# Optimization experiments

Measured on AMD Instinct MI355X. Metric: run time of the kernel, lower is better.

## Reference

```python
import jax, jax.numpy as jnp
import numpy as np

# Mamba2 defaults (mamba_ssm): expand=2, headdim=64, d_conv=4, ngroups=1
D_MODEL, D_STATE, D_INNER, HEADDIM, D_CONV = 512, 64, 1024, 64, 4
NHEADS = D_INNER // HEADDIM  # 16
CONV_DIM = D_INNER + 2 * D_STATE  # 1152
D_IN_PROJ = 2 * D_INNER + 2 * D_STATE + NHEADS  # 2192
BATCH, SEQLEN = 2, 2048
RMS_EPS = 1.1920929e-07  # torch nn.RMSNorm eps=None -> fp32 machine eps
GNORM_EPS = 1e-5  # mamba_ssm RMSNormGated default


def _rms(t, w, eps):
    return t * jax.lax.rsqrt(jnp.mean(t * t, axis=-1, keepdims=True) + eps) * w


def _mamba2(u, in_w, conv_w, conv_b, dt_bias, A_log, Dp, gnorm_w, out_w):
    """Mamba2 block forward (ngroups=1). u: (b, l, d_model) -> (b, l, d_model)."""
    b, l, _ = u.shape
    zxbcdt = jnp.einsum('bld,ed->ble', u, in_w)  # (b, l, 2192)
    z = zxbcdt[..., :D_INNER]
    xBC = zxbcdt[..., D_INNER:D_INNER + CONV_DIM]
    dt = jax.nn.softplus(zxbcdt[..., -NHEADS:] + dt_bias)  # (b, l, h)
    # causal depthwise conv, kernel D_CONV, then SiLU
    xp = jnp.pad(xBC, ((0, 0), (D_CONV - 1, 0), (0, 0)))
    xBC = conv_b + sum(xp[:, i:i + l, :] * conv_w[:, i] for i in range(D_CONV))
    xBC = jax.nn.silu(xBC)
    x = xBC[..., :D_INNER].reshape(b, l, NHEADS, HEADDIM)
    Bm = xBC[..., D_INNER:D_INNER + D_STATE]  # (b, l, n)
    Cm = xBC[..., D_INNER + D_STATE:]         # (b, l, n)
    dA = jnp.exp(dt * (-jnp.exp(A_log)))      # (b, l, h), decay per head

    def step(h, inp):
        dA_t, dt_t, B_t, C_t, x_t = inp  # (b,h) (b,h) (b,n) (b,n) (b,h,p)
        h = h * dA_t[:, :, None, None] + jnp.einsum('bh,bhp,bn->bhpn', dt_t, x_t, B_t)
        y = jnp.einsum('bhpn,bn->bhp', h, C_t)
        return h, y

    h0 = jnp.zeros((b, NHEADS, HEADDIM, D_STATE), u.dtype)
    xs = (jnp.swapaxes(dA, 0, 1), jnp.swapaxes(dt, 0, 1), jnp.swapaxes(Bm, 0, 1),
          jnp.swapaxes(Cm, 0, 1), jnp.swapaxes(x, 0, 1))
    _, ys = jax.lax.scan(step, h0, xs)  # (l, b, h, p)
    y = jnp.swapaxes(ys, 0, 1) + x * Dp[None, None, :, None]
    y = y.reshape(b, l, D_INNER)
    # gated RMSNorm: norm(y * silu(z)) * weight
    y = y * jax.nn.silu(z)
    y = _rms(y, gnorm_w, GNORM_EPS)
    return jnp.einsum('bli,oi->blo', y, out_w)


def _layer(x, pos_emb, pixel_mask, norm_ssm_w, norm_ffn_w, ffn_w1, ffn_b1, ffn_w2, ffn_b2,
           f_in_w, f_conv_w, f_conv_b, f_dt_bias, f_A_log, f_D, f_gnorm_w, f_out_w,
           b_in_w, b_conv_w, b_conv_b, b_dt_bias, b_A_log, b_D, b_gnorm_w, b_out_w):
    si = _rms(x, norm_ssm_w, RMS_EPS) + pos_emb
    fwd = _mamba2(si, f_in_w, f_conv_w, f_conv_b, f_dt_bias, f_A_log, f_D, f_gnorm_w, f_out_w)
    bwd = jnp.flip(_mamba2(jnp.flip(si, 1), b_in_w, b_conv_w, b_conv_b, b_dt_bias,
                           b_A_log, b_D, b_gnorm_w, b_out_w), 1)
    ssm_out = (fwd + bwd) * pixel_mask[..., None]  # merge='add'
    x = x + ssm_out
    h = _rms(x, norm_ffn_w, RMS_EPS)
    h = jax.nn.gelu(h @ ffn_w1.T + ffn_b1, approximate=False)
    return x + (h @ ffn_w2.T + ffn_b2)


def setup_inputs() -> dict:
    key = jax.random.key(0)
    ks = jax.random.split(key, 16)
    f32 = jnp.float32
    inp = {}
    inp['x'] = jax.random.normal(ks[0], (BATCH, SEQLEN, D_MODEL), f32)
    inp['pos_emb'] = jax.random.normal(ks[1], (BATCH, SEQLEN, D_MODEL), f32) * 0.02
    inp['pixel_mask'] = jnp.ones((BATCH, SEQLEN), f32)
    inp['norm_ssm_w'] = jnp.ones((D_MODEL,), f32)
    inp['norm_ffn_w'] = jnp.ones((D_MODEL,), f32)
    d_ffn = 4 * D_MODEL
    inp['ffn_w1'] = jax.random.normal(ks[2], (d_ffn, D_MODEL), f32) * 0.02
    inp['ffn_b1'] = jnp.zeros((d_ffn,), f32)
    inp['ffn_w2'] = jax.random.normal(ks[3], (D_MODEL, d_ffn), f32) * 0.02
    inp['ffn_b2'] = jnp.zeros((D_MODEL,), f32)
    i = 4
    for pre in ('f', 'b'):
        inp[pre + '_in_w'] = jax.random.normal(ks[i], (D_IN_PROJ, D_MODEL), f32) * 0.02; i += 1
        inp[pre + '_conv_w'] = jax.random.uniform(ks[i], (CONV_DIM, D_CONV), f32, -0.5, 0.5); i += 1
        inp[pre + '_conv_b'] = jnp.zeros((CONV_DIM,), f32)
        dt0 = jnp.exp(jax.random.uniform(ks[i], (NHEADS,), f32) * (jnp.log(0.1) - jnp.log(0.001)) + jnp.log(0.001)); i += 1
        inp[pre + '_dt_bias'] = dt0 + jnp.log(-jnp.expm1(-dt0))  # inverse softplus
        inp[pre + '_A_log'] = jnp.log(jax.random.uniform(ks[i], (NHEADS,), f32, 1.0, 16.0)); i += 1
        inp[pre + '_D'] = jnp.ones((NHEADS,), f32)
        inp[pre + '_gnorm_w'] = jnp.ones((D_INNER,), f32)
        inp[pre + '_out_w'] = jax.random.normal(ks[i], (D_MODEL, D_INNER), f32) * 0.02; i += 1
    return inp


def reference(x, pos_emb, pixel_mask, norm_ssm_w, norm_ffn_w, ffn_w1, ffn_b1, ffn_w2, ffn_b2,
              f_in_w, f_conv_w, f_conv_b, f_dt_bias, f_A_log, f_D, f_gnorm_w, f_out_w,
              b_in_w, b_conv_w, b_conv_b, b_dt_bias, b_A_log, b_D, b_gnorm_w, b_out_w):
    return _layer(x, pos_emb, pixel_mask, norm_ssm_w, norm_ffn_w, ffn_w1, ffn_b1, ffn_w2, ffn_b2,
                  f_in_w, f_conv_w, f_conv_b, f_dt_bias, f_A_log, f_D, f_gnorm_w, f_out_w,
                  b_in_w, b_conv_w, b_conv_b, b_dt_bias, b_A_log, b_D, b_gnorm_w, b_out_w)
```

## Files before the change

kernel.cpp:

```cpp
#include <hip/hip_runtime.h>
#include <hip/hip_bf16.h>

typedef unsigned short u16;
typedef unsigned int u32;
typedef __bf16 bf16x8 __attribute__((ext_vector_type(8)));
typedef float f32x4 __attribute__((ext_vector_type(4)));

typedef __attribute__((address_space(1))) void gvoid_t;
typedef __attribute__((address_space(3))) void lvoid_t;
__device__ __forceinline__ void lds_cp16(void* lds, const void* g) {
    __builtin_amdgcn_global_load_lds((gvoid_t*)g, (lvoid_t*)lds, 16, 0, 0);
}

__device__ __forceinline__ float bf2f(u16 v) {
    u32 x = (u32)v << 16;
    return __builtin_bit_cast(float, x);
}
__device__ __forceinline__ u16 f2bf(float f) {
    return __builtin_bit_cast(u16, (__bf16)f);
}

__device__ __forceinline__ float block_sum_256(float v, float* red) {
    #pragma unroll
    for (int o = 32; o > 0; o >>= 1) v += __shfl_xor(v, o);
    int w = threadIdx.x >> 6;
    if ((threadIdx.x & 63) == 0) red[w] = v;
    __syncthreads();
    return red[0] + red[1] + red[2] + red[3];
}

__global__ void k_cvt_all(const float* __restrict__ f_inw, const float* __restrict__ b_inw,
                          const float* __restrict__ f_ow, const float* __restrict__ b_ow,
                          const float* __restrict__ w1, const float* __restrict__ w2,
                          u16* __restrict__ INWF, u16* __restrict__ INWB,
                          u16* __restrict__ OWF, u16* __restrict__ OWB,
                          u16* __restrict__ W1B, u16* __restrict__ W2B) {
    int i = blockIdx.x * 256 + threadIdx.x;
    if (i < 1179648) { int n = i >> 9; INWF[i] = (n < 2192) ? f2bf(f_inw[i]) : (u16)0; return; }
    i -= 1179648;
    if (i < 1179648) { int n = i >> 9; INWB[i] = (n < 2192) ? f2bf(b_inw[i]) : (u16)0; return; }
    i -= 1179648;
    if (i < 524288) { OWF[i] = f2bf(f_ow[i]); return; }
    i -= 524288;
    if (i < 524288) { OWB[i] = f2bf(b_ow[i]); return; }
    i -= 524288;
    if (i < 1048576) { W1B[i] = f2bf(w1[i]); return; }
    i -= 1048576;
    if (i < 1048576) W2B[i] = f2bf(w2[i]);
}

__global__ __launch_bounds__(256) void k_rms_pos(const float* __restrict__ x,
                                                 const float* __restrict__ pe,
                                                 const float* __restrict__ wrms,
                                                 u16* __restrict__ sib) {
    __shared__ float red[4];
    int row = blockIdx.x, t = threadIdx.x;
    size_t base = (size_t)row * 512 + t * 2;
    float2 xv = *(const float2*)(x + base);
    float ss = block_sum_256(xv.x * xv.x + xv.y * xv.y, red);
    float sc = rsqrtf(ss * (1.f / 512.f) + 1.1920929e-07f);
    float2 pv = *(const float2*)(pe + base);
    float2 wv = *(const float2*)(wrms + t * 2);
    sib[base] = f2bf(xv.x * sc * wv.x + pv.x);
    sib[base + 1] = f2bf(xv.y * sc * wv.y + pv.y);
}

__global__ __launch_bounds__(256) void k_gemm_in(
    const u16* __restrict__ A, const u16* __restrict__ W0, const u16* __restrict__ W1,
    u16* __restrict__ Z0, u16* __restrict__ Z1,
    u16* __restrict__ XB0, u16* __restrict__ XB1) {
    const int z = blockIdx.z;
    const u16* W = z ? W1 : W0;
    u16* Z = z ? Z1 : Z0;
    u16* XB = z ? XB1 : XB0;
    const int K = 512;

    __shared__ __align__(16) u16 As[128 * 32];
    __shared__ __align__(16) u16 Bs[128 * 32];

    const int t = threadIdx.x;
    const int lane = t & 63;
    const int w = t >> 6;
    const int m0 = blockIdx.y * 128;
    const int n0 = blockIdx.x * 128;
    const int wm = (w >> 1) * 64;
    const int wn = (w & 1) * 64;
    const int fr = lane & 15;
    const int fk = (lane >> 4) * 8;

    f32x4 acc[4][4];
    #pragma unroll
    for (int i = 0; i < 4; ++i)
        #pragma unroll
        for (int j = 0; j < 4; ++j) acc[i][j] = (f32x4){0.f, 0.f, 0.f, 0.f};

    for (int kt = 0; kt < K; kt += 32) {
        #pragma unroll
        for (int j = 0; j < 2; ++j) {
            int off16 = j * 256 + t;
            int row = off16 >> 2;
            int kc = (off16 & 3) * 8;
            int gm = m0 + row;
            if (z) gm = (gm & ~2047) | (2047 - (gm & 2047));
            lds_cp16(As + off16 * 8, A + (size_t)gm * K + kt + kc);
            lds_cp16(Bs + off16 * 8, W + (size_t)(n0 + row) * K + kt + kc);
        }
        __syncthreads();
        bf16x8 af[4], bfr[4];
        #pragma unroll
        for (int i = 0; i < 4; ++i) af[i] = *(const bf16x8*)(As + (wm + i * 16 + fr) * 32 + fk);
        #pragma unroll
        for (int i = 0; i < 4; ++i) bfr[i] = *(const bf16x8*)(Bs + (wn + i * 16 + fr) * 32 + fk);
        #pragma unroll
        for (int i = 0; i < 4; ++i)
            #pragma unroll
            for (int j = 0; j < 4; ++j)
                acc[i][j] = __builtin_amdgcn_mfma_f32_16x16x32_bf16(af[i], bfr[j], acc[i][j], 0, 0, 0);
        __syncthreads();
    }
    #pragma unroll
    for (int i = 0; i < 4; ++i) {
        int rbase = m0 + wm + i * 16 + (lane >> 4) * 4;
        #pragma unroll
        for (int j = 0; j < 4; ++j) {
            int c = n0 + wn + j * 16 + fr;
            #pragma unroll
            for (int r = 0; r < 4; ++r) {
                u16 v = f2bf(acc[i][j][r]);
                int m = rbase + r;
                if (c < 1024) Z[(size_t)m * 1024 + c] = v;
                else if (c < 2192) XB[(size_t)m * 1184 + (c - 1024)] = v;
            }
        }
    }
}

template <int EPI>
__global__ __launch_bounds__(256) void k_gemm64(
    const u16* __restrict__ A0, const u16* __restrict__ A1,
    const u16* __restrict__ W0, const u16* __restrict__ W1,
    u16* __restrict__ C0, u16* __restrict__ C1, int N, int K,
    const float* __restrict__ bias, float* __restrict__ outf) {
    const int z = blockIdx.z;
    const u16* A = (EPI == 3) ? A0 : (z ? A1 : A0);
    const u16* W = (EPI == 3) ? W0 : (z ? W1 : W0);
    u16* C = z ? C1 : C0;
    int kbeg = 0, kend = K;
    if (EPI == 3) { kbeg = z * (K >> 1); kend = kbeg + (K >> 1); }

    __shared__ __align__(16) u16 As[64 * 32];
    __shared__ __align__(16) u16 Bs[64 * 32];

    const int t = threadIdx.x;
    const int lane = t & 63;
    const int w = t >> 6;
    const int m0 = blockIdx.y * 64;
    const int n0 = blockIdx.x * 64;
    const int wm = (w >> 1) * 32;
    const int wn = (w & 1) * 32;
    const int fr = lane & 15;
    const int fk = (lane >> 4) * 8;

    f32x4 acc[2][2];
    #pragma unroll
    for (int i = 0; i < 2; ++i)
        #pragma unroll
        for (int j = 0; j < 2; ++j) acc[i][j] = (f32x4){0.f, 0.f, 0.f, 0.f};

    const int srow = t >> 2;
    const int skc = (t & 3) * 8;
    for (int kt = kbeg; kt < kend; kt += 32) {
        lds_cp16(As + t * 8, A + (size_t)(m0 + srow) * K + kt + skc);
        lds_cp16(Bs + t * 8, W + (size_t)(n0 + srow) * K + kt + skc);
        __syncthreads();
        bf16x8 af[2], bfr[2];
        #pragma unroll
        for (int i = 0; i < 2; ++i) af[i] = *(const bf16x8*)(As + (wm + i * 16 + fr) * 32 + fk);
        #pragma unroll
        for (int j = 0; j < 2; ++j) bfr[j] = *(const bf16x8*)(Bs + (wn + j * 16 + fr) * 32 + fk);
        #pragma unroll
        for (int i = 0; i < 2; ++i)
            #pragma unroll
            for (int j = 0; j < 2; ++j)
                acc[i][j] = __builtin_amdgcn_mfma_f32_16x16x32_bf16(af[i], bfr[j], acc[i][j], 0, 0, 0);
        __syncthreads();
    }
    #pragma unroll
    for (int i = 0; i < 2; ++i) {
        int rbase = m0 + wm + i * 16 + (lane >> 4) * 4;
        #pragma unroll
        for (int j = 0; j < 2; ++j) {
            int col = n0 + wn + j * 16 + fr;
            #pragma unroll
            for (int r = 0; r < 4; ++r) {
                int m = rbase + r;
                float v = acc[i][j][r];
                if (EPI == 0) {
                    C[(size_t)m * N + col] = f2bf(v);
                } else if (EPI == 1) {
                    float xg = v + bias[col];
                    C[(size_t)m * N + col] = f2bf(0.5f * xg * (1.f + erff(xg * 0.70710678118654752f)));
                } else {
                    atomicAdd(outf + (size_t)m * N + col, v);
                }
            }
        }
    }
}

__global__ __launch_bounds__(160) void k_conv(
    const u16* __restrict__ xb0, const u16* __restrict__ xb1,
    const float* __restrict__ cw0, const float* __restrict__ cb0,
    const float* __restrict__ dtb0, const float* __restrict__ al0,
    const float* __restrict__ cw1, const float* __restrict__ cb1,
    const float* __restrict__ dtb1, const float* __restrict__ al1,
    u16* __restrict__ xc0, u16* __restrict__ xc1,
    float* __restrict__ dtO0, float* __restrict__ dAO0,
    float* __restrict__ dtO1, float* __restrict__ dAO1) {
    int g = blockIdx.x;
    int dir = g >> 9;
    int row0 = (g & 511) * 8;
    const u16* xb = dir ? xb1 : xb0;
    const float* cw = dir ? cw1 : cw0;
    const float* cb = dir ? cb1 : cb0;
    const float* dtb = dir ? dtb1 : dtb0;
    const float* al = dir ? al1 : al0;
    u16* xc = dir ? xc1 : xc0;
    float* dtO = dir ? dtO1 : dtO0;
    float* dAO = dir ? dAO1 : dAO0;
    int tl0 = row0 & 2047;
    int rbatch = row0 - tl0;
    int t = threadIdx.x;
    if (t < 144) {
        int col = t * 8;
        float cwa[8][4];
        #pragma unroll
        for (int j = 0; j < 8; ++j) {
            float4 c4 = *(const float4*)(cw + (col + j) * 4);
            cwa[j][0] = c4.x; cwa[j][1] = c4.y; cwa[j][2] = c4.z; cwa[j][3] = c4.w;
        }
        float cbv[8];
        float4 cb0v = *(const float4*)(cb + col);
        float4 cb1v = *(const float4*)(cb + col + 4);
        cbv[0] = cb0v.x; cbv[1] = cb0v.y; cbv[2] = cb0v.z; cbv[3] = cb0v.w;
        cbv[4] = cb1v.x; cbv[5] = cb1v.y; cbv[6] = cb1v.z; cbv[7] = cb1v.w;
        uint4 win[4];
        win[0] = win[1] = win[2] = make_uint4(0, 0, 0, 0);
        #pragma unroll
        for (int i = 0; i < 3; ++i) {
            int tt = tl0 - 3 + i;
            if (tt >= 0) win[i] = *(const uint4*)(xb + (size_t)(rbatch + tt) * 1184 + col);
        }
        for (int s = 0; s < 8; ++s) {
            win[3] = *(const uint4*)(xb + (size_t)(rbatch + tl0 + s) * 1184 + col);
            const u16* w0 = (const u16*)&win[0];
            const u16* w1 = (const u16*)&win[1];
            const u16* w2 = (const u16*)&win[2];
            const u16* w3 = (const u16*)&win[3];
            u16 ov[8];
            #pragma unroll
            for (int j = 0; j < 8; ++j) {
                float a = cbv[j] + bf2f(w0[j]) * cwa[j][0] + bf2f(w1[j]) * cwa[j][1]
                        + bf2f(w2[j]) * cwa[j][2] + bf2f(w3[j]) * cwa[j][3];
                ov[j] = f2bf(a / (1.f + expf(-a)));
            }
            *(uint4*)(xc + (size_t)(row0 + s) * 1152 + col) = *(const uint4*)ov;
            win[0] = win[1]; win[1] = win[2]; win[2] = win[3];
        }
    } else if (t < 160) {
        int hh = t - 144;
        float nal = -expf(al[hh]);
        float dtbv = dtb[hh];
        for (int s = 0; s < 8; ++s) {
            int row = row0 + s;
            float v = bf2f(xb[(size_t)row * 1184 + 1152 + hh]) + dtbv;
            float sp = (v > 20.f) ? v : log1pf(expf(v));
            dtO[row * 16 + hh] = sp;
            dAO[row * 16 + hh] = nal * sp;
        }
    }
}

__global__ __launch_bounds__(256) void k_ssd_state(
    const u16* __restrict__ xc0, const float* __restrict__ dt0, const float* __restrict__ ld0,
    const u16* __restrict__ xc1, const float* __restrict__ dt1, const float* __restrict__ ld1,
    float* __restrict__ S, float* __restrict__ Aprod) {
    int blk = blockIdx.x;
    int c = blk & 31, h = (blk >> 5) & 15, b = (blk >> 9) & 1, dir = blk >> 10;
    const u16* xc = dir ? xc1 : xc0;
    const float* dtp = dir ? dt1 : dt0;
    const float* ldp = dir ? ld1 : ld0;
    const int t = threadIdx.x, w = t >> 6, lane = t & 63;
    const int fr = lane & 15, fk = (lane >> 4) * 8;

    __shared__ __align__(16) u16 sBt[64 * 72];
    __shared__ __align__(16) u16 sXp[64 * 72];
    __shared__ float ssc[64];
    size_t row0 = (size_t)b * 2048 + c * 64;

    if (t < 64) {
        float v = ldp[(row0 + t) * 16 + h];
        float dtv = dtp[(row0 + t) * 16 + h];
        #pragma unroll
        for (int o = 1; o < 64; o <<= 1) {
            float u = __shfl_up(v, o);
            if (lane >= o) v += u;
        }
        float last = __shfl(v, 63);
        ssc[t] = dtv * expf(last - v);
        if (t == 63) Aprod[blk] = expf(v);
    }
    __syncthreads();
    #pragma unroll
    for (int i2 = t; i2 < 512; i2 += 256) {
        int r = i2 >> 3, e8 = (i2 & 7) * 8;
        size_t rb = (row0 + r) * 1152;
        uint4 bv = *(const uint4*)(xc + rb + 1024 + e8);
        uint4 xv = *(const uint4*)(xc + rb + h * 64 + e8);
        const u16* bs = (const u16*)&bv;
        const u16* xs = (const u16*)&xv;
        float sc = ssc[r];
        #pragma unroll
        for (int j = 0; j < 8; ++j) {
            sBt[(e8 + j) * 72 + r] = bs[j];
            sXp[(e8 + j) * 72 + r] = f2bf(bf2f(xs[j]) * sc);
        }
    }
    __syncthreads();

    f32x4 acc[4];
    #pragma unroll
    for (int j = 0; j < 4; ++j) acc[j] = (f32x4){0.f, 0.f, 0.f, 0.f};
    #pragma unroll
    for (int k0 = 0; k0 < 64; k0 += 32) {
        bf16x8 a = *(const bf16x8*)(sBt + (w * 16 + fr) * 72 + k0 + fk);
        #pragma unroll
        for (int j = 0; j < 4; ++j) {
            bf16x8 bb = *(const bf16x8*)(sXp + (j * 16 + fr) * 72 + k0 + fk);
            acc[j] = __builtin_amdgcn_mfma_f32_16x16x32_bf16(a, bb, acc[j], 0, 0, 0);
        }
    }
    float* Sb = S + (size_t)blk * 4096;
    int nb = w * 16 + (lane >> 4) * 4;
    #pragma unroll
    for (int j = 0; j < 4; ++j) {
        int p = j * 16 + fr;
        *(f32x4*)(Sb + p * 64 + nb) = acc[j];
    }
}

__global__ __launch_bounds__(256) void k_scan_carry(float* __restrict__ S,
                                                    const float* __restrict__ Aprod) {
    int blk = blockIdx.x;
    int t = threadIdx.x;
    float h[16];
    #pragma unroll
    for (int j = 0; j < 16; ++j) h[j] = 0.f;
    for (int c = 0; c < 32; ++c) {
        float a = Aprod[blk * 32 + c];
        float* Sp = S + ((size_t)blk * 32 + c) * 4096 + t * 16;
        float4 s0 = *(float4*)(Sp + 0), s1 = *(float4*)(Sp + 4);
        float4 s2 = *(float4*)(Sp + 8), s3 = *(float4*)(Sp + 12);
        *(float4*)(Sp + 0) = make_float4(h[0], h[1], h[2], h[3]);
        *(float4*)(Sp + 4) = make_float4(h[4], h[5], h[6], h[7]);
        *(float4*)(Sp + 8) = make_float4(h[8], h[9], h[10], h[11]);
        *(float4*)(Sp + 12) = make_float4(h[12], h[13], h[14], h[15]);
        h[0] = a * h[0] + s0.x; h[1] = a * h[1] + s0.y; h[2] = a * h[2] + s0.z; h[3] = a * h[3] + s0.w;
        h[4] = a * h[4] + s1.x; h[5] = a * h[5] + s1.y; h[6] = a * h[6] + s1.z; h[7] = a * h[7] + s1.w;
        h[8] = a * h[8] + s2.x; h[9] = a * h[9] + s2.y; h[10] = a * h[10] + s2.z; h[11] = a * h[11] + s2.w;
        h[12] = a * h[12] + s3.x; h[13] = a * h[13] + s3.y; h[14] = a * h[14] + s3.z; h[15] = a * h[15] + s3.w;
    }
}

__global__ __launch_bounds__(256) void k_ssd_y(
    const u16* __restrict__ xc0, const float* __restrict__ dt0, const float* __restrict__ ld0,
    const float* __restrict__ Dv0, u16* __restrict__ y0,
    const u16* __restrict__ xc1, const float* __restrict__ dt1, const float* __restrict__ ld1,
    const float* __restrict__ Dv1, u16* __restrict__ y1,
    const float* __restrict__ S) {
    int blk = blockIdx.x;
    int c = blk & 31, h = (blk >> 5) & 15, b = (blk >> 9) & 1, dir = blk >> 10;
    const u16* xc = dir ? xc1 : xc0;
    const float* dtp = dir ? dt1 : dt0;
    const float* ldp = dir ? ld1 : ld0;
    u16* y = dir ? y1 : y0;
    const float Dh = (dir ? Dv1 : Dv0)[h];
    const int t = threadIdx.x, w = t >> 6, lane = t & 63;
    const int fr = lane & 15, fk = (lane >> 4) * 8;

    __shared__ __align__(16) u16 sB[64 * 72];
    __shared__ __align__(16) u16 sC[64 * 72];
    __shared__ __align__(16) u16 sXp[64 * 72];
    __shared__ __align__(16) u16 sHi[64 * 72];
    __shared__ __align__(16) u16 sLo[64 * 72];
    __shared__ __align__(16) u16 sGl[64 * 72];
    __shared__ float scl[64], sdt[64];
    size_t row0 = (size_t)b * 2048 + c * 64;

    if (t < 64) {
        float v = ldp[(row0 + t) * 16 + h];
        float dtv = dtp[(row0 + t) * 16 + h];
        #pragma unroll
        for (int o = 1; o < 64; o <<= 1) {
            float u = __shfl_up(v, o);
            if (lane >= o) v += u;
        }
        scl[t] = v;
        sdt[t] = dtv;
    }
    __syncthreads();
    #pragma unroll
    for (int i2 = t; i2 < 512; i2 += 256) {
        int r = i2 >> 3, e8 = (i2 & 7) * 8;
        size_t rb = (row0 + r) * 1152;
        *(uint4*)(sB + r * 72 + e8) = *(const uint4*)(xc + rb + 1024 + e8);
        *(uint4*)(sC + r * 72 + e8) = *(const uint4*)(xc + rb + 1088 + e8);
        uint4 xv = *(const uint4*)(xc + rb + h * 64 + e8);
        const u16* xs = (const u16*)&xv;
        float dtv = sdt[r];
        #pragma unroll
        for (int j = 0; j < 8; ++j) sXp[(e8 + j) * 72 + r] = f2bf(bf2f(xs[j]) * dtv);
    }
    #pragma unroll
    for (int i4 = t; i4 < 1024; i4 += 256) {
        int p = i4 >> 4, n4 = (i4 & 15) * 4;
        float4 hv = *(const float4*)(S + (size_t)blk * 4096 + p * 64 + n4);
        ushort4 hi4, lo4;
        hi4.x = f2bf(hv.x); lo4.x = f2bf(hv.x - bf2f(hi4.x));
        hi4.y = f2bf(hv.y); lo4.y = f2bf(hv.y - bf2f(hi4.y));
        hi4.z = f2bf(hv.z); lo4.z = f2bf(hv.z - bf2f(hi4.z));
        hi4.w = f2bf(hv.w); lo4.w = f2bf(hv.w - bf2f(hi4.w));
        *(ushort4*)(sHi + p * 72 + n4) = hi4;
        *(ushort4*)(sLo + p * 72 + n4) = lo4;
    }
    __syncthreads();

    f32x4 g[4], acc2[4];
    #pragma unroll
    for (int j = 0; j < 4; ++j) { g[j] = (f32x4){0.f,0.f,0.f,0.f}; acc2[j] = (f32x4){0.f,0.f,0.f,0.f}; }
    #pragma unroll
    for (int k0 = 0; k0 < 64; k0 += 32) {
        bf16x8 a = *(const bf16x8*)(sC + (w * 16 + fr) * 72 + k0 + fk);
        #pragma unroll
        for (int j = 0; j < 4; ++j) {
            bf16x8 bb = *(const bf16x8*)(sB + (j * 16 + fr) * 72 + k0 + fk);
            g[j] = __builtin_amdgcn_mfma_f32_16x16x32_bf16(a, bb, g[j], 0, 0, 0);
            bf16x8 bh = *(const bf16x8*)(sHi + (j * 16 + fr) * 72 + k0 + fk);
            acc2[j] = __builtin_amdgcn_mfma_f32_16x16x32_bf16(a, bh, acc2[j], 0, 0, 0);
            bf16x8 bl = *(const bf16x8*)(sLo + (j * 16 + fr) * 72 + k0 + fk);
            acc2[j] = __builtin_amdgcn_mfma_f32_16x16x32_bf16(a, bl, acc2[j], 0, 0, 0);
        }
    }
    #pragma unroll
    for (int j = 0; j < 4; ++j) {
        int r = j * 16 + fr;
        #pragma unroll
        for (int reg = 0; reg < 4; ++reg) {
            int s = w * 16 + (lane >> 4) * 4 + reg;
            float val = (r <= s) ? expf(scl[s] - scl[r]) * g[j][reg] : 0.f;
            sGl[s * 72 + r] = f2bf(val);
        }
    }
    __syncthreads();

    f32x4 acc1[4];
    #pragma unroll
    for (int j = 0; j < 4; ++j) acc1[j] = (f32x4){0.f, 0.f, 0.f, 0.f};
    #pragma unroll
    for (int k0 = 0; k0 < 64; k0 += 32) {
        bf16x8 a = *(const bf16x8*)(sGl + (w * 16 + fr) * 72 + k0 + fk);
        #pragma unroll
        for (int j = 0; j < 4; ++j) {
            bf16x8 bb = *(const bf16x8*)(sXp + (j * 16 + fr) * 72 + k0 + fk);
            acc1[j] = __builtin_amdgcn_mfma_f32_16x16x32_bf16(a, bb, acc1[j], 0, 0, 0);
        }
    }
    #pragma unroll
    for (int reg = 0; reg < 4; ++reg) {
        int s = w * 16 + (lane >> 4) * 4 + reg;
        float es = expf(scl[s]);
        size_t yrb = (row0 + s) * 1024 + h * 64;
        size_t xrb = (row0 + s) * 1152 + h * 64;
        #pragma unroll
        for (int j = 0; j < 4; ++j) {
            int p = j * 16 + fr;
            float xv = bf2f(xc[xrb + p]);
            y[yrb + p] = f2bf(acc1[j][reg] + es * acc2[j][reg] + xv * Dh);
        }
    }
}

__global__ __launch_bounds__(256) void k_gnorm(
    const u16* __restrict__ y0, const u16* __restrict__ z0,
    const float* __restrict__ gw0, u16* __restrict__ o0,
    const u16* __restrict__ y1, const u16* __restrict__ z1,
    const float* __restrict__ gw1, u16* __restrict__ o1) {
    __shared__ float red[4];
    int r = blockIdx.x;
    int dir = r >> 12, row = r & 4095;
    int t = threadIdx.x;
    const u16* y = dir ? y1 : y0;
    const u16* zp = dir ? z1 : z0;
    const float* gw = dir ? gw1 : gw0;
    u16* o = dir ? o1 : o0;
    ushort4 yv = *(const ushort4*)(y + (size_t)row * 1024 + t * 4);
    ushort4 zr = *(const ushort4*)(zp + (size_t)row * 1024 + t * 4);
    float z0f = bf2f(zr.x), z1f = bf2f(zr.y), z2f = bf2f(zr.z), z3f = bf2f(zr.w);
    float v0 = bf2f(yv.x) * (z0f / (1.f + expf(-z0f)));
    float v1 = bf2f(yv.y) * (z1f / (1.f + expf(-z1f)));
    float v2 = bf2f(yv.z) * (z2f / (1.f + expf(-z2f)));
    float v3 = bf2f(yv.w) * (z3f / (1.f + expf(-z3f)));
    float ss = block_sum_256(v0 * v0 + v1 * v1 + v2 * v2 + v3 * v3, red);
    float sc = rsqrtf(ss * (1.f / 1024.f) + 1e-5f);
    float4 gv = *(const float4*)(gw + t * 4);
    size_t ob = (size_t)row * 1024 + t * 4;
    o[ob + 0] = f2bf(v0 * sc * gv.x);
    o[ob + 1] = f2bf(v1 * sc * gv.y);
    o[ob + 2] = f2bf(v2 * sc * gv.z);
    o[ob + 3] = f2bf(v3 * sc * gv.w);
}

__global__ __launch_bounds__(256) void k_add_rms(
    const float* __restrict__ x, const u16* __restrict__ of,
    const u16* __restrict__ ob, const float* __restrict__ mask,
    const float* __restrict__ wrms, const float* __restrict__ b2,
    float* __restrict__ x2, u16* __restrict__ o, float* __restrict__ outf) {
    __shared__ float red[4];
    int row = blockIdx.x, t = threadIdx.x;
    int bb = row >> 11, tl = row & 2047;
    size_t fb = (size_t)((bb << 11) + (2047 - tl)) * 512;
    float m = mask[row];
    size_t base = (size_t)row * 512 + t * 2;
    size_t fo = fb + t * 2;
    float2 xv = *(const float2*)(x + base);
    float v0 = xv.x + (bf2f(of[base]) + bf2f(ob[fo])) * m;
    float v1 = xv.y + (bf2f(of[base + 1]) + bf2f(ob[fo + 1])) * m;
    x2[base] = v0;
    x2[base + 1] = v1;
    float2 b2v = *(const float2*)(b2 + t * 2);
    outf[base] = v0 + b2v.x;
    outf[base + 1] = v1 + b2v.y;
    float ss = block_sum_256(v0 * v0 + v1 * v1, red);
    float sc = rsqrtf(ss * (1.f / 512.f) + 1.1920929e-07f);
    float2 wv = *(const float2*)(wrms + t * 2);
    o[base] = f2bf(v0 * sc * wv.x);
    o[base + 1] = f2bf(v1 * sc * wv.y);
}

extern "C" void kernel_launch(void* const* d_in, const int* in_sizes, int n_in,
                              void* d_out, int out_size, void* d_ws, size_t ws_size,
                              hipStream_t stream) {
    const float* x = (const float*)d_in[0];
    const float* pe = (const float*)d_in[1];
    const float* mask = (const float*)d_in[2];
    const float* nsw = (const float*)d_in[3];
    const float* nfw = (const float*)d_in[4];
    const float* w1 = (const float*)d_in[5];
    const float* b1 = (const float*)d_in[6];
    const float* w2 = (const float*)d_in[7];
    const float* b2 = (const float*)d_in[8];
    const float* f_inw = (const float*)d_in[9];
    const float* f_cw = (const float*)d_in[10];
    const float* f_cb = (const float*)d_in[11];
    const float* f_dtb = (const float*)d_in[12];
    const float* f_al = (const float*)d_in[13];
    const float* f_D = (const float*)d_in[14];
    const float* f_gw = (const float*)d_in[15];
    const float* f_ow = (const float*)d_in[16];
    const float* b_inw = (const float*)d_in[17];
    const float* b_cw = (const float*)d_in[18];
    const float* b_cb = (const float*)d_in[19];
    const float* b_dtb = (const float*)d_in[20];
    const float* b_al = (const float*)d_in[21];
    const float* b_D = (const float*)d_in[22];
    const float* b_gw = (const float*)d_in[23];
    const float* b_ow = (const float*)d_in[24];
    float* out = (float*)d_out;

    char* ws = (char*)d_ws;
    u16* Z0   = (u16*)(ws + 0);
    u16* Z1   = (u16*)(ws + 8388608);
    u16* XB0  = (u16*)(ws + 16777216);
    u16* XB1  = (u16*)(ws + 26476544);
    u16* INWF = (u16*)(ws + 36175872);
    u16* INWB = (u16*)(ws + 38535168);
    u16* SIB  = (u16*)(ws + 40894464);
    u16* XC0  = (u16*)(ws + 36175872);
    u16* XC1  = (u16*)(ws + 45613056);
    float* dtF = (float*)(ws + 55050240);
    float* dAF = (float*)(ws + 55312384);
    float* dtB = (float*)(ws + 55574528);
    float* dAB = (float*)(ws + 55836672);
    u16* Y0   = (u16*)(ws + 16777216);
    u16* Y1   = (u16*)(ws + 25165824);
    u16* YG0  = (u16*)(ws + 36175872);
    u16* YG1  = (u16*)(ws + 44564480);
    u16* OP0  = (u16*)(ws + 0);
    u16* OP1  = (u16*)(ws + 4194304);
    float* X2 = (float*)(ws + 8388608);
    u16* X2B  = (u16*)(ws + 0);
    u16* HACT = (u16*)(ws + 16777216);
    u16* OWF = (u16*)(ws + 56098816);
    u16* OWB = (u16*)(ws + 57147392);
    u16* W1B = (u16*)(ws + 58195968);
    u16* W2B = (u16*)(ws + 60293120);
    float* SBUF = (float*)(ws + 62390272);
    float* APR  = (float*)(ws + 95944704);

    k_cvt_all<<<21504, 256, 0, stream>>>(f_inw, b_inw, f_ow, b_ow, w1, w2,
                                         INWF, INWB, OWF, OWB, W1B, W2B);
    k_rms_pos<<<4096, 256, 0, stream>>>(x, pe, nsw, SIB);
    k_gemm_in<<<dim3(18, 32, 2), 256, 0, stream>>>(SIB, INWF, INWB, Z0, Z1, XB0, XB1);
    k_conv<<<1024, 160, 0, stream>>>(XB0, XB1, f_cw, f_cb, f_dtb, f_al,
                                     b_cw, b_cb, b_dtb, b_al,
                                     XC0, XC1, dtF, dAF, dtB, dAB);
    k_ssd_state<<<2048, 256, 0, stream>>>(XC0, dtF, dAF, XC1, dtB, dAB, SBUF, APR);
    k_scan_carry<<<64, 256, 0, stream>>>(SBUF, APR);
    k_ssd_y<<<2048, 256, 0, stream>>>(XC0, dtF, dAF, f_D, Y0,
                                      XC1, dtB, dAB, b_D, Y1, SBUF);
    k_gnorm<<<8192, 256, 0, stream>>>(Y0, Z0, f_gw, YG0, Y1, Z1, b_gw, YG1);
    k_gemm64<0><<<dim3(8, 64, 2), 256, 0, stream>>>(YG0, YG1, OWF, OWB, OP0, OP1, 512, 1024,
                                                    nullptr, nullptr);
    k_add_rms<<<4096, 256, 0, stream>>>(x, OP0, OP1, mask, nfw, b2, X2, X2B, out);
    k_gemm64<1><<<dim3(32, 64, 1), 256, 0, stream>>>(X2B, X2B, W1B, W1B, HACT, HACT, 2048, 512,
                                                     b1, nullptr);
    k_gemm64<3><<<dim3(8, 64, 2), 256, 0, stream>>>(HACT, HACT, W2B, W2B, nullptr, nullptr,
                                                    512, 2048, nullptr, out);
}
```

Measured before the change: 353.1 us.

## Merge prep kernels, deepen in-proj GEMM K tile, parallelize chunk carry scan

Fuses the weight conversion and RMS/pos-embedding kernels into one launch to save a launch and a tail. Doubles the K tile of the input projection GEMM to 64, halving barriers per K step at the cost of more LDS. Rewrites the inter-chunk state carry so each thread owns one state element across 32 chunks, launching 1024 blocks instead of 64 and preloading all chunk values to expose memory parallelism.

```diff
diff --git a/kernel.cpp b/kernel.cpp
--- a/kernel.cpp
+++ b/kernel.cpp
@@ -29,32 +29,32 @@
     return red[0] + red[1] + red[2] + red[3];
 }
 
-__global__ void k_cvt_all(const float* __restrict__ f_inw, const float* __restrict__ b_inw,
-                          const float* __restrict__ f_ow, const float* __restrict__ b_ow,
-                          const float* __restrict__ w1, const float* __restrict__ w2,
-                          u16* __restrict__ INWF, u16* __restrict__ INWB,
-                          u16* __restrict__ OWF, u16* __restrict__ OWB,
-                          u16* __restrict__ W1B, u16* __restrict__ W2B) {
-    int i = blockIdx.x * 256 + threadIdx.x;
-    if (i < 1179648) { int n = i >> 9; INWF[i] = (n < 2192) ? f2bf(f_inw[i]) : (u16)0; return; }
-    i -= 1179648;
-    if (i < 1179648) { int n = i >> 9; INWB[i] = (n < 2192) ? f2bf(b_inw[i]) : (u16)0; return; }
-    i -= 1179648;
-    if (i < 524288) { OWF[i] = f2bf(f_ow[i]); return; }
-    i -= 524288;
-    if (i < 524288) { OWB[i] = f2bf(b_ow[i]); return; }
-    i -= 524288;
-    if (i < 1048576) { W1B[i] = f2bf(w1[i]); return; }
-    i -= 1048576;
-    if (i < 1048576) W2B[i] = f2bf(w2[i]);
-}
-
-__global__ __launch_bounds__(256) void k_rms_pos(const float* __restrict__ x,
-                                                 const float* __restrict__ pe,
-                                                 const float* __restrict__ wrms,
-                                                 u16* __restrict__ sib) {
+__global__ __launch_bounds__(256) void k_prep(
+    const float* __restrict__ f_inw, const float* __restrict__ b_inw,
+    const float* __restrict__ f_ow, const float* __restrict__ b_ow,
+    const float* __restrict__ w1, const float* __restrict__ w2,
+    u16* __restrict__ INWF, u16* __restrict__ INWB,
+    u16* __restrict__ OWF, u16* __restrict__ OWB,
+    u16* __restrict__ W1B, u16* __restrict__ W2B,
+    const float* __restrict__ x, const float* __restrict__ pe,
+    const float* __restrict__ wrms, u16* __restrict__ sib) {
+    if (blockIdx.x < 21504) {
+        int i = blockIdx.x * 256 + threadIdx.x;
+        if (i < 1179648) { int n = i >> 9; INWF[i] = (n < 2192) ? f2bf(f_inw[i]) : (u16)0; return; }
+        i -= 1179648;
+        if (i < 1179648) { int n = i >> 9; INWB[i] = (n < 2192) ? f2bf(b_inw[i]) : (u16)0; return; }
+        i -= 1179648;
+        if (i < 524288) { OWF[i] = f2bf(f_ow[i]); return; }
+        i -= 524288;
+        if (i < 524288) { OWB[i] = f2bf(b_ow[i]); return; }
+        i -= 524288;
+        if (i < 1048576) { W1B[i] = f2bf(w1[i]); return; }
+        i -= 1048576;
+        if (i < 1048576) W2B[i] = f2bf(w2[i]);
+        return;
+    }
     __shared__ float red[4];
-    int row = blockIdx.x, t = threadIdx.x;
+    int row = blockIdx.x - 21504, t = threadIdx.x;
     size_t base = (size_t)row * 512 + t * 2;
     float2 xv = *(const float2*)(x + base);
     float ss = block_sum_256(xv.x * xv.x + xv.y * xv.y, red);
@@ -75,8 +75,8 @@
     u16* XB = z ? XB1 : XB0;
     const int K = 512;
 
-    __shared__ __align__(16) u16 As[128 * 32];
-    __shared__ __align__(16) u16 Bs[128 * 32];
+    __shared__ __align__(16) u16 As[128 * 64];
+    __shared__ __align__(16) u16 Bs[128 * 64];
 
     const int t = threadIdx.x;
     const int lane = t & 63;
@@ -94,28 +94,31 @@
         #pragma unroll
         for (int j = 0; j < 4; ++j) acc[i][j] = (f32x4){0.f, 0.f, 0.f, 0.f};
 
-    for (int kt = 0; kt < K; kt += 32) {
-        #pragma unroll
-        for (int j = 0; j < 2; ++j) {
+    for (int kt = 0; kt < K; kt += 64) {
+        #pragma unroll
+        for (int j = 0; j < 4; ++j) {
             int off16 = j * 256 + t;
-            int row = off16 >> 2;
-            int kc = (off16 & 3) * 8;
+            int row = off16 >> 3;
+            int kc = (off16 & 7) * 8;
             int gm = m0 + row;
             if (z) gm = (gm & ~2047) | (2047 - (gm & 2047));
             lds_cp16(As + off16 * 8, A + (size_t)gm * K + kt + kc);
             lds_cp16(Bs + off16 * 8, W + (size_t)(n0 + row) * K + kt + kc);
         }
         __syncthreads();
-        bf16x8 af[4], bfr[4];
-        #pragma unroll
-        for (int i = 0; i < 4; ++i) af[i] = *(const bf16x8*)(As + (wm + i * 16 + fr) * 32 + fk);
-        #pragma unroll
-        for (int i = 0; i < 4; ++i) bfr[i] = *(const bf16x8*)(Bs + (wn + i * 16 + fr) * 32 + fk);
-        #pragma unroll
-        for (int i = 0; i < 4; ++i)
+        #pragma unroll
+        for (int k0 = 0; k0 < 64; k0 += 32) {
+            bf16x8 af[4], bfr[4];
             #pragma unroll
-            for (int j = 0; j < 4; ++j)
-                acc[i][j] = __builtin_amdgcn_mfma_f32_16x16x32_bf16(af[i], bfr[j], acc[i][j], 0, 0, 0);
+            for (int i = 0; i < 4; ++i) af[i] = *(const bf16x8*)(As + (wm + i * 16 + fr) * 64 + k0 + fk);
+            #pragma unroll
+            for (int i = 0; i < 4; ++i) bfr[i] = *(const bf16x8*)(Bs + (wn + i * 16 + fr) * 64 + k0 + fk);
+            #pragma unroll
+            for (int i = 0; i < 4; ++i)
+                #pragma unroll
+                for (int j = 0; j < 4; ++j)
+                    acc[i][j] = __builtin_amdgcn_mfma_f32_16x16x32_bf16(af[i], bfr[j], acc[i][j], 0, 0, 0);
+        }
         __syncthreads();
     }
     #pragma unroll
@@ -351,24 +354,21 @@
 
 __global__ __launch_bounds__(256) void k_scan_carry(float* __restrict__ S,
                                                     const float* __restrict__ Aprod) {
-    int blk = blockIdx.x;
-    int t = threadIdx.x;
-    float h[16];
-    #pragma unroll
-    for (int j = 0; j < 16; ++j) h[j] = 0.f;
+    int g = blockIdx.x;
+    int blk = g >> 4;
+    int e = (g & 15) * 256 + threadIdx.x;
+    size_t base = (size_t)blk * 32 * 4096 + e;
+    float sv[32];
+    #pragma unroll
+    for (int c = 0; c < 32; ++c) sv[c] = S[base + (size_t)c * 4096];
+    float ap[32];
+    #pragma unroll
+    for (int c = 0; c < 32; ++c) ap[c] = Aprod[blk * 32 + c];
+    float h = 0.f;
+    #pragma unroll
     for (int c = 0; c < 32; ++c) {
-        float a = Aprod[blk * 32 + c];
-        float* Sp = S + ((size_t)blk * 32 + c) * 4096 + t * 16;
-        float4 s0 = *(float4*)(Sp + 0), s1 = *(float4*)(Sp + 4);
-        float4 s2 = *(float4*)(Sp + 8), s3 = *(float4*)(Sp + 12);
-        *(float4*)(Sp + 0) = make_float4(h[0], h[1], h[2], h[3]);
-        *(float4*)(Sp + 4) = make_float4(h[4], h[5], h[6], h[7]);
-        *(float4*)(Sp + 8) = make_float4(h[8], h[9], h[10], h[11]);
-        *(float4*)(Sp + 12) = make_float4(h[12], h[13], h[14], h[15]);
-        h[0] = a * h[0] + s0.x; h[1] = a * h[1] + s0.y; h[2] = a * h[2] + s0.z; h[3] = a * h[3] + s0.w;
-        h[4] = a * h[4] + s1.x; h[5] = a * h[5] + s1.y; h[6] = a * h[6] + s1.z; h[7] = a * h[7] + s1.w;
-        h[8] = a * h[8] + s2.x; h[9] = a * h[9] + s2.y; h[10] = a * h[10] + s2.z; h[11] = a * h[11] + s2.w;
-        h[12] = a * h[12] + s3.x; h[13] = a * h[13] + s3.y; h[14] = a * h[14] + s3.z; h[15] = a * h[15] + s3.w;
+        S[base + (size_t)c * 4096] = h;
+        h = ap[c] * h + sv[c];
     }
 }
 
@@ -607,15 +607,15 @@
     float* SBUF = (float*)(ws + 62390272);
     float* APR  = (float*)(ws + 95944704);
 
-    k_cvt_all<<<21504, 256, 0, stream>>>(f_inw, b_inw, f_ow, b_ow, w1, w2,
-                                         INWF, INWB, OWF, OWB, W1B, W2B);
-    k_rms_pos<<<4096, 256, 0, stream>>>(x, pe, nsw, SIB);
+    k_prep<<<25600, 256, 0, stream>>>(f_inw, b_inw, f_ow, b_ow, w1, w2,
+                                      INWF, INWB, OWF, OWB, W1B, W2B,
+                                      x, pe, nsw, SIB);
     k_gemm_in<<<dim3(18, 32, 2), 256, 0, stream>>>(SIB, INWF, INWB, Z0, Z1, XB0, XB1);
     k_conv<<<1024, 160, 0, stream>>>(XB0, XB1, f_cw, f_cb, f_dtb, f_al,
                                      b_cw, b_cb, b_dtb, b_al,
                                      XC0, XC1, dtF, dAF, dtB, dAB);
     k_ssd_state<<<2048, 256, 0, stream>>>(XC0, dtF, dAF, XC1, dtB, dAB, SBUF, APR);
-    k_scan_carry<<<64, 256, 0, stream>>>(SBUF, APR);
+    k_scan_carry<<<1024, 256, 0, stream>>>(SBUF, APR);
     k_ssd_y<<<2048, 256, 0, stream>>>(XC0, dtF, dAF, f_D, Y0,
                                       XC1, dtB, dAB, b_D, Y1, SBUF);
     k_gnorm<<<8192, 256, 0, stream>>>(Y0, Z0, f_gw, YG0, Y1, Z1, b_gw, YG1);
```

New measurement: 344.3 us. 2.5% less time.
